# Optimization experiments

Measured on AMD Instinct MI355X. Metric: run time of the kernel, lower is better.

The kernel has to match this reference:

```python
import jax, jax.numpy as jnp
import numpy as np

B, N, C = 8, 2048, 512


def setup_inputs() -> dict:
    key = jax.random.key(0)
    ks = jax.random.split(key, 8)
    s = 1.0 / np.sqrt(C)
    return {
        "x": jax.random.normal(ks[0], (B, N, C), dtype=jnp.float32),
        "Wq": jax.random.normal(ks[1], (C, C), dtype=jnp.float32) * s,
        "Wk": jax.random.normal(ks[2], (C, C), dtype=jnp.float32) * s,
        "Wv": jax.random.normal(ks[3], (C, C), dtype=jnp.float32) * s,
        "W1": jax.random.normal(ks[4], (C, C), dtype=jnp.float32) * s,
        "W2": jax.random.normal(ks[5], (C, C), dtype=jnp.float32) * s,
        "gamma": jax.random.normal(ks[6], (1,), dtype=jnp.float32),
        "beta_p": jax.random.normal(ks[7], (1,), dtype=jnp.float32),
    }


def reference(x, Wq, Wk, Wv, W1, W2, gamma, beta_p):
    # torch.nn.Linear(bias=False): y = x @ W.T  with W of shape [out, in]
    q = jnp.einsum('bnc,dc->bnd', x, Wq)  # [B,N,C]
    k = jnp.einsum('bnc,dc->bnd', x, Wk)
    v = jnp.einsum('bnc,dc->bnd', x, Wv)
    # scores[b,i,j] = q_i . k_j ; softmax over dim=1 (the i axis), as in source
    scores = jnp.einsum('bic,bjc->bij', q, k)        # [B,N,N]
    attn = jax.nn.softmax(scores, axis=1)            # normalize over i
    # bmm(v^T, attn): out[b,c,j] = sum_i v[b,i,c] * attn[b,i,j]; permuted back -> [B,N,C]
    att_out = jnp.einsum('bic,bij->bjc', v, attn)    # [B,N,C]
    o = gamma * att_out + x                          # gamma-scaled residual
    h = jax.nn.relu(jnp.einsum('bnc,dc->bnd', o, W1))
    o = beta_p * jnp.einsum('bnc,dc->bnd', h, W2) + o
    return o
```

## Files before the change

kernel.cpp:

```cpp
#include <hip/hip_runtime.h>
#include <stdint.h>

#define DEVINL __device__ __forceinline__

typedef short short8_t __attribute__((ext_vector_type(8)));
typedef float f32x4_t  __attribute__((ext_vector_type(4)));
typedef _Float16 half8_t __attribute__((ext_vector_type(8)));
typedef unsigned short u16;

static constexpr int  Bn = 8;
static constexpr int  Nn = 2048;
static constexpr int  Cn = 512;
static constexpr int  Mn = Bn * Nn;
static constexpr long NC = (long)Nn * Cn;
static constexpr long NNe = (long)Nn * Nn;
static constexpr long CC = (long)Cn * Cn;
static constexpr long MC = (long)Mn * Cn;

DEVINL u16 f32_to_f16(float f) {
  _Float16 h = (_Float16)f;
  u16 r; __builtin_memcpy(&r, &h, 2);
  return r;
}

DEVINL void mfma_f16(f32x4_t& d, short8_t a, short8_t b) {
  asm("v_mfma_f32_16x16x32_f16 %0, %1, %2, %0" : "+v"(d) : "v"(a), "v"(b));
}

#define GLOAD_LDS16(G, L)                                                      \
  __builtin_amdgcn_global_load_lds(                                            \
      (const __attribute__((address_space(1))) void*)(G),                      \
      (__attribute__((address_space(3))) void*)(L), 16, 0, 0)

__global__ __launch_bounds__(256) void conv_x_kernel(const float* __restrict__ src,
                                                     u16* __restrict__ f16, int n4) {
  int i = blockIdx.x * 256 + threadIdx.x;
  if (i >= n4) return;
  float4 v = ((const float4*)src)[i];
  ((ushort4*)f16)[i] = make_ushort4(f32_to_f16(v.x), f32_to_f16(v.y),
                                    f32_to_f16(v.z), f32_to_f16(v.w));
}

struct W5 { const float* p[5]; };
__global__ __launch_bounds__(256) void conv_w_kernel(W5 ws, u16* __restrict__ f16,
                                                     int n4each) {
  const int w = blockIdx.y;
  const int i = blockIdx.x * 256 + threadIdx.x;
  if (i >= n4each) return;
  float4 v = ((const float4*)ws.p[w])[i];
  ((ushort4*)f16)[(long)w * (CC / 4) + i] =
      make_ushort4(f32_to_f16(v.x), f32_to_f16(v.y), f32_to_f16(v.z), f32_to_f16(v.w));
}

enum { EPI_QKV = 0, EPI_SF16 = 2, EPI_PV = 3, EPI_RELU = 4, EPI_FFN2 = 5 };

template <int BN, int EPI, int SW>
__global__ __launch_bounds__(512, 2) void gemm_k(
    const u16* Ah, const u16* Bh,
    int K, int outld, void* out0, void* out1,
    const float* aux, const float* scal,
    int batch0, long azStride, long bzStride, long ozStride) {
  constexpr int BM = 256, BK = 64;
  constexpr int FM = (BN == 256) ? 8 : 4;
  constexpr int FN = 4;
  constexpr int BISS = BN / 64;
  constexpr int ABYTES = BM * BK * 2;
  constexpr int BBYTES = BN * BK * 2;
  constexpr int PB = ABYTES + BBYTES;

  __shared__ __align__(1024) char lds[2 * PB];

  const int tid = threadIdx.x;
  const int l   = tid & 63;
  const int wid = tid >> 6;

  int bx, byy, bz;
  {
    const int gx = gridDim.x, gy = gridDim.y, gz = gridDim.z;
    const int lid = blockIdx.x + gx * (blockIdx.y + gy * blockIdx.z);
    if (SW == 0) {
      const int c = lid & 7, s = lid >> 3;
      const int nyz = gy * gz;
      const int xi = s / nyz, yz = s - xi * nyz;
      bx = c + 8 * xi; byy = yz % gy; bz = yz / gy;
    } else if (SW == 1) {
      bz = lid & 7;
      const int s = lid >> 3;
      byy = s % gy; bx = s / gy;
    } else {
      bx = blockIdx.x; byy = blockIdx.y; bz = blockIdx.z;
    }
  }

  const int batch = batch0 + bz;
  const int brow  = bx * BM;
  const int bcol  = byy * BN;

  Ah += (long)bz * azStride;
  Bh += (long)bz * bzStride;

  const int wrL  = (BN == 256) ? (wid >> 2) * 128 : (wid >> 1) * 64;
  const int wcL  = (BN == 256) ? (wid & 3) * 64   : (wid & 1) * 64;
  const int rsel = l & 15;

  f32x4_t acc[FM][FN];
  const f32x4_t zero = {0.f, 0.f, 0.f, 0.f};
#pragma unroll
  for (int m = 0; m < FM; ++m)
#pragma unroll
    for (int n = 0; n < FN; ++n) acc[m][n] = zero;

  const int cb = ((l & 7) ^ ((l >> 3) & 7)) * 8;
  auto stageA = [&](int k0, char* dst) {
#pragma unroll
    for (int j = 0; j < 4; ++j) {
      const int rr = (wid * 4 + j) * 8 + (l >> 3);
      GLOAD_LDS16(Ah + (long)(brow + rr) * K + (k0 + cb), dst + (wid * 4 + j) * 1024);
    }
  };
  auto stageB = [&](int k0, char* dst) {
#pragma unroll
    for (int j = 0; j < BISS; ++j) {
      const int rr = (wid * BISS + j) * 8 + (l >> 3);
      GLOAD_LDS16(Bh + (long)(bcol + rr) * K + (k0 + cb), dst + (wid * BISS + j) * 1024);
    }
  };
  auto stageAll = [&](int k0, char* b) { stageA(k0, b); stageB(k0, b + ABYTES); };

  auto rdA = [&](const char* bufA, int m, int ks) -> short8_t {
    const int r = wrL + m * 16 + rsel;
    const int s = ks * 4 + (l >> 4);
    return *(const short8_t*)(bufA + r * 128 + ((s ^ (r & 7)) << 4));
  };
  auto rdB = [&](const char* bufB, int n, int ks) -> short8_t {
    const int r = wcL + n * 16 + rsel;
    const int s = ks * 4 + (l >> 4);
    return *(const short8_t*)(bufB + r * 128 + ((s ^ (r & 7)) << 4));
  };

  const int NT = K >> 6;
  stageAll(0, lds);
  for (int kt = 0; kt < NT; ++kt) {
    const char* bb = lds + (kt & 1) * PB;
    if (kt + 1 < NT) {
      stageAll((kt + 1) << 6, lds + ((kt + 1) & 1) * PB);
      __builtin_amdgcn_sched_barrier(0);
      if constexpr (BN == 256)
        asm volatile("s_waitcnt vmcnt(8)" ::: "memory");
      else
        asm volatile("s_waitcnt vmcnt(6)" ::: "memory");
    } else {
      __builtin_amdgcn_sched_barrier(0);
      asm volatile("s_waitcnt vmcnt(0)" ::: "memory");
    }
    __builtin_amdgcn_sched_barrier(0);
    __builtin_amdgcn_s_barrier();
    asm volatile("" ::: "memory");
    __builtin_amdgcn_sched_barrier(0);

    short8_t bf[FN][2];
#pragma unroll
    for (int n = 0; n < FN; ++n)
#pragma unroll
      for (int ks = 0; ks < 2; ++ks) bf[n][ks] = rdB(bb + ABYTES, n, ks);

    __builtin_amdgcn_s_setprio(1);
#pragma unroll
    for (int m = 0; m < FM; ++m) {
      short8_t a0 = rdA(bb, m, 0);
      short8_t a1 = rdA(bb, m, 1);
#pragma unroll
      for (int n = 0; n < FN; ++n) {
        mfma_f16(acc[m][n], a0, bf[n][0]);
        mfma_f16(acc[m][n], a1, bf[n][1]);
      }
    }
    __builtin_amdgcn_s_setprio(0);

    __builtin_amdgcn_sched_barrier(0);
    asm volatile("" ::: "memory");
    __builtin_amdgcn_s_barrier();
    __builtin_amdgcn_sched_barrier(0);
  }

  const float sc0 = scal ? scal[0] : 0.0f;
  const int crow = (l >> 4) * 4;
  const int ccol = l & 15;

  if (EPI == EPI_QKV && bcol >= 1024) {
    constexpr int TPV = 264;
    u16* t = (u16*)lds;
    const long b = brow >> 11;
#pragma unroll
    for (int pass = 0; pass < 2; ++pass) {
      __syncthreads();
      if (((wid & 3) >> 1) == pass) {
        const int clBase = wcL - pass * 128;
#pragma unroll
        for (int m = 0; m < FM; ++m)
#pragma unroll
          for (int n = 0; n < FN; ++n) {
            ushort4 pk = make_ushort4(
                f32_to_f16(acc[m][n][0]), f32_to_f16(acc[m][n][1]),
                f32_to_f16(acc[m][n][2]), f32_to_f16(acc[m][n][3]));
            *(ushort4*)&t[(clBase + n * 16 + ccol) * TPV + (wrL + m * 16 + crow)] = pk;
          }
      }
      __syncthreads();
      const int colq = tid >> 2, qf = tid & 3;
      const int cv = bcol - 1024 + pass * 128 + colq;
      u16* dst = (u16*)out1 + ((b * Cn + cv) * (long)Nn + (brow & 2047) + qf * 64);
      const u16* srcT = &t[colq * TPV + qf * 64];
#pragma unroll
      for (int i = 0; i < 8; ++i)
        ((uint4*)dst)[i] = *(const uint4*)(srcT + i * 8);
    }
    return;
  }

#pragma unroll
  for (int m = 0; m < FM; ++m)
#pragma unroll
    for (int n = 0; n < FN; ++n)
#pragma unroll
      for (int j = 0; j < 4; ++j) {
        const int r = brow + wrL + m * 16 + crow + j;
        const int c = bcol + wcL + n * 16 + ccol;
        const float v = acc[m][n][j];
        if (EPI == EPI_QKV) {
          ((u16*)out0)[(long)(c >> 9) * MC + (long)r * Cn + (c & 511)] = f32_to_f16(v);
        } else if (EPI == EPI_SF16) {
          ((u16*)out0 + (long)bz * ozStride)[(long)r * outld + c] = f32_to_f16(v);
        } else if (EPI == EPI_PV) {
          const long gi = ((long)batch * Nn + r) * Cn + c;
          const float val = sc0 * v + aux[gi];
          ((float*)out0)[gi] = val;
          ((u16*)out1)[gi] = f32_to_f16(val);
        } else if (EPI == EPI_RELU) {
          const float val = v > 0.f ? v : 0.f;
          ((u16*)out0)[(long)r * outld + c] = f32_to_f16(val);
        } else {
          const long gi = (long)r * Cn + c;
          ((float*)out0)[gi] = sc0 * v + aux[gi];
        }
      }
}

__global__ __launch_bounds__(256) void softmax_k(const u16* sc, u16* attn) {
  const long base = (long)blockIdx.y * NNe + (long)blockIdx.x * Nn;
  const int tid = threadIdx.x;
  const int l = tid & 63, wid = tid >> 6;
  half8_t v = ((const half8_t*)(sc + base))[tid];
  float f[8];
#pragma unroll
  for (int i = 0; i < 8; ++i) f[i] = (float)v[i];
  float mx = f[0];
#pragma unroll
  for (int i = 1; i < 8; ++i) mx = fmaxf(mx, f[i]);
#pragma unroll
  for (int o = 32; o > 0; o >>= 1) mx = fmaxf(mx, __shfl_xor(mx, o));
  __shared__ float red[8];
  if (l == 0) red[wid] = mx;
  __syncthreads();
  mx = fmaxf(fmaxf(red[0], red[1]), fmaxf(red[2], red[3]));
  float p[8];
  float s = 0.f;
#pragma unroll
  for (int i = 0; i < 8; ++i) { p[i] = __expf(f[i] - mx); s += p[i]; }
#pragma unroll
  for (int o = 32; o > 0; o >>= 1) s += __shfl_xor(s, o);
  if (l == 0) red[4 + wid] = s;
  __syncthreads();
  s = red[4] + red[5] + red[6] + red[7];
  const float inv = 1.0f / s;
  __align__(16) u16 o8[8];
#pragma unroll
  for (int i = 0; i < 8; ++i) o8[i] = f32_to_f16(p[i] * inv);
  ((uint4*)(attn + base))[tid] = *(const uint4*)o8;
}

extern "C" void kernel_launch(void* const* d_in, const int* in_sizes, int n_in,
                              void* d_out, int out_size, void* d_ws, size_t ws_size,
                              hipStream_t stream) {
  const float* x  = (const float*)d_in[0];
  const float* gamma = (const float*)d_in[6];
  const float* beta  = (const float*)d_in[7];
  float* out = (float*)d_out;

  char* ws = (char*)d_ws;
  size_t off = 0;
  auto alloc = [&](size_t bytes) {
    char* p = ws + off;
    off += (bytes + 1023) & ~(size_t)1023;
    return p;
  };
  u16* x16  = (u16*)alloc((size_t)MC * 2);
  u16* w16A = (u16*)alloc((size_t)5 * CC * 2);
  u16* qk16 = (u16*)alloc((size_t)2 * MC * 2);
  u16* vT   = (u16*)alloc((size_t)MC * 2);
  u16* o16  = (u16*)alloc((size_t)MC * 2);
  u16* h16  = (u16*)alloc((size_t)MC * 2);
  const size_t baseOff = off;

  int zAtt = 8;
  while (zAtt > 1 &&
         baseOff + (size_t)zAtt * (NNe * 2 + 1024 + NNe * 2 + 1024) > ws_size)
    zAtt >>= 1;
  u16* scoresT = (u16*)alloc((size_t)zAtt * NNe * 2);
  u16* attnT   = (u16*)alloc((size_t)zAtt * NNe * 2);
  u16* q16 = qk16;
  u16* k16 = qk16 + (size_t)MC;

  conv_x_kernel<<<dim3(MC / 4 / 256), 256, 0, stream>>>(x, x16, MC / 4);
  W5 w5 = {{(const float*)d_in[1], (const float*)d_in[2], (const float*)d_in[3],
            (const float*)d_in[4], (const float*)d_in[5]}};
  conv_w_kernel<<<dim3(CC / 4 / 256, 5), 256, 0, stream>>>(w5, w16A, CC / 4);

  gemm_k<256,EPI_QKV,0><<<dim3(Mn/256, 1536/256, 1), 512, 0, stream>>>(
      x16, w16A, Cn, Cn, qk16, vT, nullptr, nullptr, 0, 0, 0, 0);

  if (zAtt == 8) {
    gemm_k<256,EPI_SF16,1><<<dim3(Nn/256, Nn/256, 8), 512, 0, stream>>>(
        k16, q16, Cn, Nn, scoresT, nullptr, nullptr, nullptr, 0, NC, NC, NNe);
    softmax_k<<<dim3(Nn, 8), 256, 0, stream>>>(scoresT, attnT);
    gemm_k<128,EPI_PV,1><<<dim3(Nn/256, Cn/128, 8), 512, 0, stream>>>(
        attnT, vT, Nn, Cn, out, o16, x, gamma, 0, NNe, NC, 0);
  } else {
    for (int b0 = 0; b0 < Bn; b0 += zAtt) {
      gemm_k<256,EPI_SF16,2><<<dim3(Nn/256, Nn/256, zAtt), 512, 0, stream>>>(
          k16 + (long)b0 * NC, q16 + (long)b0 * NC,
          Cn, Nn, scoresT, nullptr, nullptr, nullptr, b0, NC, NC, NNe);
      softmax_k<<<dim3(Nn, zAtt), 256, 0, stream>>>(scoresT, attnT);
      gemm_k<128,EPI_PV,2><<<dim3(Nn/256, Cn/128, zAtt), 512, 0, stream>>>(
          attnT, vT + (long)b0 * NC, Nn, Cn, out, o16, x, gamma,
          b0, NNe, NC, 0);
    }
  }

  gemm_k<128,EPI_RELU,0><<<dim3(Mn/256, Cn/128, 1), 512, 0, stream>>>(
      o16, w16A + 3 * CC, Cn, Cn, h16, nullptr, nullptr, nullptr, 0, 0, 0, 0);
  gemm_k<128,EPI_FFN2,0><<<dim3(Mn/256, Cn/128, 1), 512, 0, stream>>>(
      h16, w16A + 4 * CC, Cn, Cn, out, nullptr, out, beta, 0, 0, 0, 0);
}
```

Measured before the change: 233.3 us.

## Read fp16 residuals instead of fp32 and use narrower QKV tiles

```diff
diff --git a/kernel.cpp b/kernel.cpp
--- a/kernel.cpp
+++ b/kernel.cpp
@@ -21,6 +21,10 @@
   _Float16 h = (_Float16)f;
   u16 r; __builtin_memcpy(&r, &h, 2);
   return r;
+}
+DEVINL float f16_to_f32(u16 h) {
+  _Float16 v; __builtin_memcpy(&v, &h, 2);
+  return (float)v;
 }
 
 DEVINL void mfma_f16(f32x4_t& d, short8_t a, short8_t b) {
@@ -58,7 +62,7 @@
 __global__ __launch_bounds__(512, 2) void gemm_k(
     const u16* Ah, const u16* Bh,
     int K, int outld, void* out0, void* out1,
-    const float* aux, const float* scal,
+    const void* aux, const float* scal,
     int batch0, long azStride, long bzStride, long ozStride) {
   constexpr int BM = 256, BK = 64;
   constexpr int FM = (BN == 256) ? 8 : 4;
@@ -192,29 +196,21 @@
     u16* t = (u16*)lds;
     const long b = brow >> 11;
 #pragma unroll
-    for (int pass = 0; pass < 2; ++pass) {
-      __syncthreads();
-      if (((wid & 3) >> 1) == pass) {
-        const int clBase = wcL - pass * 128;
-#pragma unroll
-        for (int m = 0; m < FM; ++m)
-#pragma unroll
-          for (int n = 0; n < FN; ++n) {
-            ushort4 pk = make_ushort4(
-                f32_to_f16(acc[m][n][0]), f32_to_f16(acc[m][n][1]),
-                f32_to_f16(acc[m][n][2]), f32_to_f16(acc[m][n][3]));
-            *(ushort4*)&t[(clBase + n * 16 + ccol) * TPV + (wrL + m * 16 + crow)] = pk;
-          }
+    for (int m = 0; m < FM; ++m)
+#pragma unroll
+      for (int n = 0; n < FN; ++n) {
+        ushort4 pk = make_ushort4(f32_to_f16(acc[m][n][0]), f32_to_f16(acc[m][n][1]),
+                                  f32_to_f16(acc[m][n][2]), f32_to_f16(acc[m][n][3]));
+        *(ushort4*)&t[(wcL + n * 16 + ccol) * TPV + (wrL + m * 16 + crow)] = pk;
       }
-      __syncthreads();
-      const int colq = tid >> 2, qf = tid & 3;
-      const int cv = bcol - 1024 + pass * 128 + colq;
-      u16* dst = (u16*)out1 + ((b * Cn + cv) * (long)Nn + (brow & 2047) + qf * 64);
-      const u16* srcT = &t[colq * TPV + qf * 64];
-#pragma unroll
-      for (int i = 0; i < 8; ++i)
-        ((uint4*)dst)[i] = *(const uint4*)(srcT + i * 8);
-    }
+    __syncthreads();
+    const int colq = tid >> 2, qf = tid & 3;
+    const int cv = bcol - 1024 + colq;
+    u16* dst = (u16*)out1 + ((b * Cn + cv) * (long)Nn + (brow & 2047) + qf * 64);
+    const u16* srcT = &t[colq * TPV + qf * 64];
+#pragma unroll
+    for (int i = 0; i < 8; ++i)
+      ((uint4*)dst)[i] = *(const uint4*)(srcT + i * 8);
     return;
   }
 
@@ -233,15 +229,15 @@
           ((u16*)out0 + (long)bz * ozStride)[(long)r * outld + c] = f32_to_f16(v);
         } else if (EPI == EPI_PV) {
           const long gi = ((long)batch * Nn + r) * Cn + c;
-          const float val = sc0 * v + aux[gi];
-          ((float*)out0)[gi] = val;
-          ((u16*)out1)[gi] = f32_to_f16(val);
+          const float xa = f16_to_f32(((const u16*)aux)[gi]);
+          ((u16*)out1)[gi] = f32_to_f16(sc0 * v + xa);
         } else if (EPI == EPI_RELU) {
           const float val = v > 0.f ? v : 0.f;
           ((u16*)out0)[(long)r * outld + c] = f32_to_f16(val);
         } else {
           const long gi = (long)r * Cn + c;
-          ((float*)out0)[gi] = sc0 * v + aux[gi];
+          const float oa = f16_to_f32(((const u16*)aux)[gi]);
+          ((float*)out0)[gi] = sc0 * v + oa;
         }
       }
 }
@@ -316,7 +312,7 @@
             (const float*)d_in[4], (const float*)d_in[5]}};
   conv_w_kernel<<<dim3(CC / 4 / 256, 5), 256, 0, stream>>>(w5, w16A, CC / 4);
 
-  gemm_k<256,EPI_QKV,0><<<dim3(Mn/256, 1536/256, 1), 512, 0, stream>>>(
+  gemm_k<128,EPI_QKV,0><<<dim3(Mn/256, 1536/128, 1), 512, 0, stream>>>(
       x16, w16A, Cn, Cn, qk16, vT, nullptr, nullptr, 0, 0, 0, 0);
 
   if (zAtt == 8) {
@@ -324,7 +320,7 @@
         k16, q16, Cn, Nn, scoresT, nullptr, nullptr, nullptr, 0, NC, NC, NNe);
     softmax_k<<<dim3(Nn, 8), 256, 0, stream>>>(scoresT, attnT);
     gemm_k<128,EPI_PV,1><<<dim3(Nn/256, Cn/128, 8), 512, 0, stream>>>(
-        attnT, vT, Nn, Cn, out, o16, x, gamma, 0, NNe, NC, 0);
+        attnT, vT, Nn, Cn, nullptr, o16, x16, gamma, 0, NNe, NC, 0);
   } else {
     for (int b0 = 0; b0 < Bn; b0 += zAtt) {
       gemm_k<256,EPI_SF16,2><<<dim3(Nn/256, Nn/256, zAtt), 512, 0, stream>>>(
@@ -332,7 +328,7 @@
           Cn, Nn, scoresT, nullptr, nullptr, nullptr, b0, NC, NC, NNe);
       softmax_k<<<dim3(Nn, zAtt), 256, 0, stream>>>(scoresT, attnT);
       gemm_k<128,EPI_PV,2><<<dim3(Nn/256, Cn/128, zAtt), 512, 0, stream>>>(
-          attnT, vT + (long)b0 * NC, Nn, Cn, out, o16, x, gamma,
+          attnT, vT + (long)b0 * NC, Nn, Cn, nullptr, o16, x16, gamma,
           b0, NNe, NC, 0);
     }
   }
@@ -340,5 +336,5 @@
   gemm_k<128,EPI_RELU,0><<<dim3(Mn/256, Cn/128, 1), 512, 0, stream>>>(
       o16, w16A + 3 * CC, Cn, Cn, h16, nullptr, nullptr, nullptr, 0, 0, 0, 0);
   gemm_k<128,EPI_FFN2,0><<<dim3(Mn/256, Cn/128, 1), 512, 0, stream>>>(
-      h16, w16A + 4 * CC, Cn, Cn, out, nullptr, out, beta, 0, 0, 0, 0);
-}
+      h16, w16A + 4 * CC, Cn, Cn, out, nullptr, o16, beta, 0, 0, 0, 0);
+}
```

Result: faster. 205.1 us (-12.1%).
